# Kernel tuning notes

Hardware: AMD Instinct MI355X
Metric: run time of the kernel (lower is better)

The kernel has to match this reference:

```python
import jax, jax.numpy as jnp
import numpy as np
import math

B, S, E, H = 2, 2048, 1024, 16
D = E // H  # head_dim = 64
WINDOW = 512
EPS = 1e-5


def _layernorm(x, gamma, beta):
    mu = jnp.mean(x, axis=-1, keepdims=True)
    var = jnp.var(x, axis=-1, keepdims=True)
    return (x - mu) * jax.lax.rsqrt(var + EPS) * gamma + beta


def setup_inputs() -> dict:
    key = jax.random.key(0)
    ks = jax.random.split(key, 5)
    return {
        "x": jax.random.normal(ks[0], (B, S, E), jnp.float32),
        "W_qkv": jax.random.normal(ks[1], (E, 3 * E), jnp.float32) * (E ** -0.5),
        "b_qkv": jax.random.normal(ks[2], (3 * E,), jnp.float32) * 0.02,
        "q_gamma": jnp.ones((D,), jnp.float32),
        "q_beta": jnp.zeros((D,), jnp.float32),
        "k_gamma": jnp.ones((D,), jnp.float32),
        "k_beta": jnp.zeros((D,), jnp.float32),
        "W_out": jax.random.normal(ks[3], (E, E), jnp.float32) * (E ** -0.5),
        "b_out": jax.random.normal(ks[4], (E,), jnp.float32) * 0.02,
    }


def reference(x, W_qkv, b_qkv, q_gamma, q_beta, k_gamma, k_beta, W_out, b_out):
    b, s, e = x.shape
    # fused QKV projection -> (3, B, H, S, D)
    qkv = (x @ W_qkv + b_qkv).reshape(b, s, 3, H, D).transpose(2, 0, 3, 1, 4)
    q, k, v = qkv[0], qkv[1], qkv[2]
    # qk_norm: LayerNorm over head_dim
    q = _layernorm(q, q_gamma, q_beta)
    k = _layernorm(k, k_gamma, k_beta)
    scores = jnp.einsum("bhqd,bhkd->bhqk", q, k) / math.sqrt(D)
    # causal + sliding-window mask (True = masked out)
    row = jnp.arange(s)[:, None]
    col = jnp.arange(s)[None, :]
    masked = (col > row) | (row - col >= WINDOW)  # sliding window subsumes causal
    scores = jnp.where(masked[None, None], -jnp.inf, scores)
    attn = jax.nn.softmax(scores, axis=-1)
    out = jnp.einsum("bhqk,bhkd->bhqd", attn, v)  # (B,H,S,D)
    out = out.transpose(0, 2, 1, 3).reshape(b, s, e)
    return out @ W_out + b_out
```

## Files before the change

### kernel.cpp

```cpp
#include <hip/hip_runtime.h>
#include <stdint.h>

typedef uint16_t u16;
typedef __attribute__((ext_vector_type(8))) short short8;
typedef __attribute__((ext_vector_type(4))) float f32x4;

#define DEV static __device__ __forceinline__

DEV u16 f2bf(float f) {
  uint32_t u = __float_as_uint(f);
  return (u16)((u + 0x7fffu + ((u >> 16) & 1u)) >> 16);
}
DEV float bf2f(u16 h) { return __uint_as_float(((uint32_t)h) << 16); }

DEV void gload16(const void* g, void* l) {
  __builtin_amdgcn_global_load_lds(
      (const __attribute__((address_space(1))) void*)g,
      (__attribute__((address_space(3))) void*)l, 16, 0, 0);
}

__global__ void k_cast4(const float* __restrict__ in, u16* __restrict__ out, int n4) {
  int i = blockIdx.x * blockDim.x + threadIdx.x;
  if (i >= n4) return;
  float4 v = ((const float4*)in)[i];
  uint2 p;
  p.x = (uint32_t)f2bf(v.x) | ((uint32_t)f2bf(v.y) << 16);
  p.y = (uint32_t)f2bf(v.z) | ((uint32_t)f2bf(v.w) << 16);
  ((uint2*)out)[i] = p;
}

__global__ void k_tcast(const float* __restrict__ Wm, u16* __restrict__ Wt, int K, int N) {
  __shared__ u16 t[64][65];
  int n0 = blockIdx.x * 64, k0 = blockIdx.y * 64;
  int tid = threadIdx.x;
#pragma unroll
  for (int i = 0; i < 16; ++i) {
    int idx = tid + i * 256, r = idx >> 6, c = idx & 63;
    t[r][c] = f2bf(Wm[(size_t)(k0 + r) * N + n0 + c]);
  }
  __syncthreads();
#pragma unroll
  for (int i = 0; i < 16; ++i) {
    int idx = tid + i * 256, r = idx >> 6, c = idx & 63;
    Wt[(size_t)(n0 + r) * K + k0 + c] = t[c][r];
  }
}

__global__ __launch_bounds__(512) void k_gemmqkv8(
    const u16* __restrict__ A, const u16* __restrict__ Bt,
    const float* __restrict__ bias,
    const float* __restrict__ qg, const float* __restrict__ qb,
    const float* __restrict__ kg, const float* __restrict__ kb,
    u16* __restrict__ Qn, u16* __restrict__ Kn, u16* __restrict__ Vt) {
  const int K = 1024, N = 3072;
  __shared__ __attribute__((aligned(16))) u16 SA[2][16384];
  __shared__ __attribute__((aligned(16))) u16 SB[2][16384];
  int bid = blockIdx.x;
  int ntn = N >> 8;
  int cpx = gridDim.x >> 3;
  int wg = (bid & 7) * cpx + (bid >> 3);
  int my = wg / ntn, nx = wg - my * ntn;
  int m0 = my * 256, n0 = nx * 256;
  int tid = threadIdx.x, lane = tid & 63, w = tid >> 6;
  int wm = w >> 2, wn = w & 3;
  int wr = wm * 128, wc = wn * 64;
  int lr = lane & 15, lg = lane >> 4;
  int rsw = (lr & 7) << 3;
  int srow = tid >> 3;
  int scb = ((tid & 7) ^ ((tid >> 3) & 7)) * 8;
  f32x4 acc[8][4];
#pragma unroll
  for (int i = 0; i < 8; ++i)
#pragma unroll
    for (int j = 0; j < 4; ++j) acc[i][j] = (f32x4){0.f, 0.f, 0.f, 0.f};

  int nk = K >> 6;

#define STG8(buf, kt)                                                                    \
  do {                                                                                   \
    gload16(A + (size_t)(m0 + srow) * K + (kt) * 64 + scb, &SA[buf][tid * 8]);           \
    gload16(A + (size_t)(m0 + 64 + srow) * K + (kt) * 64 + scb, &SA[buf][4096 + tid * 8]);   \
    gload16(A + (size_t)(m0 + 128 + srow) * K + (kt) * 64 + scb, &SA[buf][8192 + tid * 8]);  \
    gload16(A + (size_t)(m0 + 192 + srow) * K + (kt) * 64 + scb, &SA[buf][12288 + tid * 8]); \
    gload16(Bt + (size_t)(n0 + srow) * K + (kt) * 64 + scb, &SB[buf][tid * 8]);          \
    gload16(Bt + (size_t)(n0 + 64 + srow) * K + (kt) * 64 + scb, &SB[buf][4096 + tid * 8]);  \
    gload16(Bt + (size_t)(n0 + 128 + srow) * K + (kt) * 64 + scb, &SB[buf][8192 + tid * 8]); \
    gload16(Bt + (size_t)(n0 + 192 + srow) * K + (kt) * 64 + scb, &SB[buf][12288 + tid * 8]); \
  } while (0)

  STG8(0, 0);
  STG8(1, 1);

  for (int t = 0; t < nk; ++t) {
    int cur = t & 1;
    if (t + 1 < nk)
      asm volatile("s_waitcnt vmcnt(8)" ::: "memory");
    else
      asm volatile("s_waitcnt vmcnt(0)" ::: "memory");
    __syncthreads();
#pragma unroll
    for (int ks = 0; ks < 2; ++ks) {
      short8 bfr[4];
#pragma unroll
      for (int ni = 0; ni < 4; ++ni)
        bfr[ni] = *(const short8*)&SB[cur][((wc + ni * 16 + lr) * 64 + ks * 32 + lg * 8) ^ rsw];
#pragma unroll
      for (int mh = 0; mh < 2; ++mh) {
        short8 afr[4];
#pragma unroll
        for (int a = 0; a < 4; ++a)
          afr[a] = *(const short8*)&SA[cur][((wr + (mh * 4 + a) * 16 + lr) * 64 + ks * 32 + lg * 8) ^ rsw];
        __builtin_amdgcn_s_setprio(1);
#pragma unroll
        for (int a = 0; a < 4; ++a)
#pragma unroll
          for (int ni = 0; ni < 4; ++ni)
            acc[mh * 4 + a][ni] =
                __builtin_amdgcn_mfma_f32_16x16x32_bf16(afr[a], bfr[ni], acc[mh * 4 + a][ni], 0, 0, 0);
        __builtin_amdgcn_s_setprio(0);
      }
    }
    __syncthreads();
    if (t + 2 < nk) STG8(cur, t + 2);
  }
#undef STG8

  int sec = n0 >> 10;
  int hh = ((n0 + wc) >> 6) & 15;
  int b = m0 >> 11;
  int s0 = m0 & 2047;

  if (sec < 2) {
    const float* gp = sec ? kg : qg;
    const float* bp = sec ? kb : qb;
    float scl = sec ? 1.f : (0.125f * 1.44269504f);
    u16* op = sec ? Kn : Qn;
    float gv[4], bev[4], bb[4];
#pragma unroll
    for (int ni = 0; ni < 4; ++ni) {
      int d = ni * 16 + lr;
      gv[ni] = gp[d];
      bev[ni] = bp[d];
      bb[ni] = bias[n0 + wc + d];
    }
    size_t hb = (size_t)(b * 16 + hh) * 2048 * 64;
#pragma unroll
    for (int mi = 0; mi < 8; ++mi) {
      float a[4][4], ps[4], ps2[4];
#pragma unroll
      for (int ni = 0; ni < 4; ++ni)
#pragma unroll
        for (int j = 0; j < 4; ++j) a[ni][j] = acc[mi][ni][j] + bb[ni];
#pragma unroll
      for (int j = 0; j < 4; ++j) {
        ps[j] = a[0][j] + a[1][j] + a[2][j] + a[3][j];
        ps2[j] = a[0][j] * a[0][j] + a[1][j] * a[1][j] + a[2][j] * a[2][j] + a[3][j] * a[3][j];
      }
#pragma unroll
      for (int m = 1; m < 16; m <<= 1)
#pragma unroll
        for (int j = 0; j < 4; ++j) {
          ps[j] += __shfl_xor(ps[j], m, 64);
          ps2[j] += __shfl_xor(ps2[j], m, 64);
        }
#pragma unroll
      for (int j = 0; j < 4; ++j) {
        float mean = ps[j] * (1.f / 64);
        float var = ps2[j] * (1.f / 64) - mean * mean;
        float r = rsqrtf(var + 1e-5f);
        int row = s0 + wr + mi * 16 + lg * 4 + j;
        size_t base = hb + (size_t)row * 64;
#pragma unroll
        for (int ni = 0; ni < 4; ++ni) {
          float v = ((a[ni][j] - mean) * r * gv[ni] + bev[ni]) * scl;
          op[base + ni * 16 + lr] = f2bf(v);
        }
      }
    }
  } else {
    u16* vbase = Vt + (size_t)(b * 16 + hh) * 64 * 2048;
#pragma unroll
    for (int ni = 0; ni < 4; ++ni) {
      int d = ni * 16 + lr;
      float bb = bias[n0 + wc + d];
#pragma unroll
      for (int mi = 0; mi < 8; ++mi) {
        int row0 = s0 + wr + mi * 16 + lg * 4;
        uint2 pk;
        pk.x = (uint32_t)f2bf(acc[mi][ni][0] + bb) | ((uint32_t)f2bf(acc[mi][ni][1] + bb) << 16);
        pk.y = (uint32_t)f2bf(acc[mi][ni][2] + bb) | ((uint32_t)f2bf(acc[mi][ni][3] + bb) << 16);
        *(uint2*)(vbase + (size_t)d * 2048 + row0) = pk;
      }
    }
  }
}

template <int OUT_BF16>
__global__ __launch_bounds__(256) void k_gemm4(
    const u16* __restrict__ A, const u16* __restrict__ Bt,
    const float* __restrict__ bias, void* __restrict__ Cout,
    int M, int N, int K) {
  __shared__ __attribute__((aligned(16))) u16 S[2][2][128 * 64];
  int bid = blockIdx.x;
  int ntn = N >> 7;
  int cpx = gridDim.x >> 3;
  int wg = (bid & 7) * cpx + (bid >> 3);
  int my = wg / ntn, nx = wg - my * ntn;
  int m0 = my * 128, n0 = nx * 128;
  int tid = threadIdx.x, lane = tid & 63, w = tid >> 6;
  int wr = (w >> 1) * 64, wc = (w & 1) * 64;
  int lr = lane & 15, lg = lane >> 4;
  int rsw = (lr & 7) << 3;
  int srow = tid >> 3;
  int scb = ((tid & 7) ^ ((tid >> 3) & 7)) * 8;
  f32x4 acc[4][4];
#pragma unroll
  for (int i = 0; i < 4; ++i)
#pragma unroll
    for (int j = 0; j < 4; ++j) acc[i][j] = (f32x4){0.f, 0.f, 0.f, 0.f};

  int nk = K >> 6;

#define STG4(buf, kt)                                                                   \
  do {                                                                                  \
    gload16(A + (size_t)(m0 + srow) * K + (kt) * 64 + scb, &S[buf][0][tid * 8]);        \
    gload16(A + (size_t)(m0 + 32 + srow) * K + (kt) * 64 + scb, &S[buf][0][2048 + tid * 8]);  \
    gload16(A + (size_t)(m0 + 64 + srow) * K + (kt) * 64 + scb, &S[buf][0][4096 + tid * 8]);  \
    gload16(A + (size_t)(m0 + 96 + srow) * K + (kt) * 64 + scb, &S[buf][0][6144 + tid * 8]);  \
    gload16(Bt + (size_t)(n0 + srow) * K + (kt) * 64 + scb, &S[buf][1][tid * 8]);       \
    gload16(Bt + (size_t)(n0 + 32 + srow) * K + (kt) * 64 + scb, &S[buf][1][2048 + tid * 8]); \
    gload16(Bt + (size_t)(n0 + 64 + srow) * K + (kt) * 64 + scb, &S[buf][1][4096 + tid * 8]); \
    gload16(Bt + (size_t)(n0 + 96 + srow) * K + (kt) * 64 + scb, &S[buf][1][6144 + tid * 8]); \
  } while (0)

  STG4(0, 0);
  asm volatile("s_waitcnt vmcnt(0)" ::: "memory");
  __syncthreads();

  for (int t = 0; t < nk; ++t) {
    int cur = t & 1;
    if (t + 1 < nk) STG4(cur ^ 1, t + 1);
#pragma unroll
    for (int ks = 0; ks < 2; ++ks) {
      short8 af[4], bf[4];
#pragma unroll
      for (int mi = 0; mi < 4; ++mi)
        af[mi] = *(const short8*)&S[cur][0][((wr + mi * 16 + lr) * 64 + ks * 32 + lg * 8) ^ rsw];
#pragma unroll
      for (int ni = 0; ni < 4; ++ni)
        bf[ni] = *(const short8*)&S[cur][1][((wc + ni * 16 + lr) * 64 + ks * 32 + lg * 8) ^ rsw];
      __builtin_amdgcn_s_setprio(1);
#pragma unroll
      for (int mi = 0; mi < 4; ++mi)
#pragma unroll
        for (int ni = 0; ni < 4; ++ni)
          acc[mi][ni] = __builtin_amdgcn_mfma_f32_16x16x32_bf16(af[mi], bf[ni], acc[mi][ni], 0, 0, 0);
      __builtin_amdgcn_s_setprio(0);
    }
    asm volatile("s_waitcnt vmcnt(0)" ::: "memory");
    __syncthreads();
  }
#undef STG4

  int rg = lg * 4;
#pragma unroll
  for (int mi = 0; mi < 4; ++mi) {
#pragma unroll
    for (int ni = 0; ni < 4; ++ni) {
      int col = n0 + wc + ni * 16 + lr;
      float bv = bias[col];
#pragma unroll
      for (int j = 0; j < 4; ++j) {
        int row = m0 + wr + mi * 16 + rg + j;
        float o = acc[mi][ni][j] + bv;
        if (OUT_BF16) ((u16*)Cout)[(size_t)row * N + col] = f2bf(o);
        else ((float*)Cout)[(size_t)row * N + col] = o;
      }
    }
  }
}

__global__ __launch_bounds__(256) void k_attn7(
    const u16* __restrict__ Qn, const u16* __restrict__ Kn,
    const u16* __restrict__ Vt, u16* __restrict__ attb) {
  __shared__ __attribute__((aligned(16))) u16 KL[2][4096];
  __shared__ __attribute__((aligned(16))) u16 VL[2][4096];
  __shared__ __attribute__((aligned(16))) u16 Pl[4][2304];
  int bid = blockIdx.x;
  int xcd = bid & 7, idx = bid >> 3;
  int bh = xcd * 4 + (idx & 3);
  int qb = 15 - (idx >> 2);
  int q0 = qb * 128;
  int tid = threadIdx.x, lane = tid & 63, w = tid >> 6;
  int ln15 = lane & 15, lg = lane >> 4;
  int qlo = q0 + w * 32;
  const u16* Qh = Qn + (size_t)bh * (2048 * 64);
  const u16* Kh = Kn + (size_t)bh * (2048 * 64);
  const u16* Vh = Vt + (size_t)bh * (64 * 2048);
  int rsw = (ln15 & 7) << 3;
  int srow = tid >> 3;
  int scb = ((tid & 7) ^ ((tid >> 3) & 7)) * 8;

  short8 qf[2][2];
#pragma unroll
  for (int qs = 0; qs < 2; ++qs)
#pragma unroll
    for (int h2 = 0; h2 < 2; ++h2)
      qf[qs][h2] = *(const short8*)(Qh + (size_t)(qlo + qs * 16 + ln15) * 64 + h2 * 32 + lg * 8);

  f32x4 oacc[2][4];
#pragma unroll
  for (int qs = 0; qs < 2; ++qs)
#pragma unroll
    for (int dt = 0; dt < 4; ++dt) oacc[qs][dt] = (f32x4){0.f, 0.f, 0.f, 0.f};
  float lwp[2][4];
#pragma unroll
  for (int qs = 0; qs < 2; ++qs)
#pragma unroll
    for (int j = 0; j < 4; ++j) lwp[qs][j] = 0.f;

  int t0 = q0 >= 512 ? (q0 - 511) >> 6 : 0;
  int t1 = (q0 + 127) >> 6;

#define STAGE_A7(buf, kt)                                                              \
  do {                                                                                 \
    const u16* Kt_ = Kh + (size_t)(kt) * 4096;                                         \
    gload16(Kt_ + (size_t)srow * 64 + scb, &KL[buf][tid * 8]);                         \
    gload16(Kt_ + (size_t)(srow + 32) * 64 + scb, &KL[buf][2048 + tid * 8]);           \
    const u16* Vt_ = Vh + (size_t)(kt) * 64;                                           \
    gload16(Vt_ + (size_t)srow * 2048 + scb, &VL[buf][tid * 8]);                       \
    gload16(Vt_ + (size_t)(srow + 32) * 2048 + scb, &VL[buf][2048 + tid * 8]);         \
  } while (0)

  STAGE_A7(0, t0);
  asm volatile("s_waitcnt vmcnt(0)" ::: "memory");
  __syncthreads();

  for (int t = t0; t <= t1; ++t) {
    int cur = (t - t0) & 1;
    if (t + 1 <= t1) STAGE_A7(cur ^ 1, t + 1);
    int kt6 = t * 64;
    if (kt6 <= qlo + 31 && kt6 + 63 >= qlo - 511) {
      short8 kf[4][2];
#pragma unroll
      for (int c = 0; c < 4; ++c)
#pragma unroll
        for (int h2 = 0; h2 < 2; ++h2)
          kf[c][h2] = *(const short8*)&KL[cur][((c * 16 + ln15) * 64 + h2 * 32 + lg * 8) ^ rsw];
      f32x4 sf[2][4];
      __builtin_amdgcn_s_setprio(1);
#pragma unroll
      for (int qs = 0; qs < 2; ++qs)
#pragma unroll
        for (int c = 0; c < 4; ++c) {
          f32x4 z = (f32x4){0.f, 0.f, 0.f, 0.f};
          z = __builtin_amdgcn_mfma_f32_16x16x32_bf16(qf[qs][0], kf[c][0], z, 0, 0, 0);
          sf[qs][c] = __builtin_amdgcn_mfma_f32_16x16x32_bf16(qf[qs][1], kf[c][1], z, 0, 0, 0);
        }
      __builtin_amdgcn_s_setprio(0);
      bool interior = (kt6 + 63 <= qlo) && (kt6 >= qlo - 480);
      if (interior) {
#pragma unroll
        for (int qs = 0; qs < 2; ++qs)
#pragma unroll
          for (int c = 0; c < 4; ++c)
#pragma unroll
            for (int j = 0; j < 4; ++j) {
              float p = __builtin_amdgcn_exp2f(sf[qs][c][j]);
              sf[qs][c][j] = p;
              lwp[qs][j] += p;
            }
      } else {
#pragma unroll
        for (int qs = 0; qs < 2; ++qs)
#pragma unroll
          for (int c = 0; c < 4; ++c) {
            int kk = kt6 + c * 16 + ln15;
#pragma unroll
            for (int j = 0; j < 4; ++j) {
              int q = qlo + qs * 16 + lg * 4 + j;
              bool msk = (kk > q) || ((q - kk) >= 512);
              float p = __builtin_amdgcn_exp2f(msk ? -1e30f : sf[qs][c][j]);
              sf[qs][c][j] = p;
              lwp[qs][j] += p;
            }
          }
      }
#pragma unroll
      for (int qs = 0; qs < 2; ++qs)
#pragma unroll
        for (int c = 0; c < 4; ++c)
#pragma unroll
          for (int j = 0; j < 4; ++j) {
            uint32_t u = __float_as_uint(sf[qs][c][j]);
            Pl[w][(qs * 16 + lg * 4 + j) * 72 + c * 16 + ln15] = (u16)((u + 0x8000u) >> 16);
          }
      short8 vf[4][2];
#pragma unroll
      for (int dt = 0; dt < 4; ++dt)
#pragma unroll
        for (int h2 = 0; h2 < 2; ++h2)
          vf[dt][h2] = *(const short8*)&VL[cur][((dt * 16 + ln15) * 64 + h2 * 32 + lg * 8) ^ rsw];
      __builtin_amdgcn_s_setprio(1);
#pragma unroll
      for (int qs = 0; qs < 2; ++qs)
#pragma unroll
        for (int h2 = 0; h2 < 2; ++h2) {
          short8 pf = *(const short8*)&Pl[w][(qs * 16 + ln15) * 72 + h2 * 32 + lg * 8];
#pragma unroll
          for (int dt = 0; dt < 4; ++dt)
            oacc[qs][dt] = __builtin_amdgcn_mfma_f32_16x16x32_bf16(pf, vf[dt][h2], oacc[qs][dt], 0, 0, 0);
        }
      __builtin_amdgcn_s_setprio(0);
    }
    asm volatile("s_waitcnt vmcnt(0)" ::: "memory");
    __syncthreads();
  }
#undef STAGE_A7

  int b = bh >> 4, hh = bh & 15;
#pragma unroll
  for (int qs = 0; qs < 2; ++qs)
#pragma unroll
    for (int j = 0; j < 4; ++j) {
      float rs = lwp[qs][j];
#pragma unroll
      for (int m = 8; m > 0; m >>= 1) rs += __shfl_xor(rs, m, 64);
      float inv = rs > 0.f ? 1.f / rs : 0.f;
      int row = b * 2048 + qlo + qs * 16 + lg * 4 + j;
#pragma unroll
      for (int dt = 0; dt < 4; ++dt)
        attb[(size_t)row * 1024 + hh * 64 + dt * 16 + ln15] = f2bf(oacc[qs][dt][j] * inv);
    }
}

extern "C" void kernel_launch(void* const* d_in, const int* in_sizes, int n_in,
                              void* d_out, int out_size, void* d_ws, size_t ws_size,
                              hipStream_t stream) {
  const float* x = (const float*)d_in[0];
  const float* Wqkv = (const float*)d_in[1];
  const float* bqkv = (const float*)d_in[2];
  const float* qg = (const float*)d_in[3];
  const float* qb = (const float*)d_in[4];
  const float* kg = (const float*)d_in[5];
  const float* kb = (const float*)d_in[6];
  const float* Wout = (const float*)d_in[7];
  const float* bout = (const float*)d_in[8];
  float* out = (float*)d_out;

  char* ws = (char*)d_ws;
  u16* attb = (u16*)(ws);
  u16* Vt = (u16*)(ws + 8388608);
  u16* Qn = (u16*)(ws + 16777216);
  u16* Kn = (u16*)(ws + 25165824);
  u16* xb = (u16*)(ws + 33554432);
  u16* wqkvT = (u16*)(ws + 41943040);
  u16* woutT = (u16*)(ws + 48234496);

  k_cast4<<<4096, 256, 0, stream>>>(x, xb, 4194304 / 4);
  k_tcast<<<dim3(48, 16), 256, 0, stream>>>(Wqkv, wqkvT, 1024, 3072);
  k_tcast<<<dim3(16, 16), 256, 0, stream>>>(Wout, woutT, 1024, 1024);
  k_gemmqkv8<<<192, 512, 0, stream>>>(xb, wqkvT, bqkv, qg, qb, kg, kb, Qn, Kn, Vt);
  k_attn7<<<512, 256, 0, stream>>>(Qn, Kn, Vt, attb);
  k_gemm4<0><<<256, 256, 0, stream>>>(attb, woutT, bout, out, 4096, 1024, 1024);
}
```

Before: 100.7 us.

## Restructure QKV GEMM main loop into 8-phase ping-pong pipeline

Replaces the simple double-buffered k-loop of the fused QKV GEMM with a hand-scheduled pipeline. Each k-tile is split into four quadrant MFMA phases. Shared-memory fragment loads, split global-to-LDS loads and raw s_barrier plus lgkmcnt waits are interleaved between the phases. The aim is to overlap memory traffic with MFMA work and hide barrier latency better. In exchange it adds many more barriers and hard-coded vmcnt counts, and buffer-reuse ordering races are a real risk.

```diff
diff --git a/kernel.cpp b/kernel.cpp
--- a/kernel.cpp
+++ b/kernel.cpp
@@ -46,7 +46,7 @@
   }
 }
 
-__global__ __launch_bounds__(512) void k_gemmqkv8(
+__global__ __launch_bounds__(512) void k_gemmqkv8p(
     const u16* __restrict__ A, const u16* __restrict__ Bt,
     const float* __restrict__ bias,
     const float* __restrict__ qg, const float* __restrict__ qb,
@@ -74,56 +74,84 @@
 #pragma unroll
     for (int j = 0; j < 4; ++j) acc[i][j] = (f32x4){0.f, 0.f, 0.f, 0.f};
 
-  int nk = K >> 6;
-
-#define STG8(buf, kt)                                                                    \
-  do {                                                                                   \
-    gload16(A + (size_t)(m0 + srow) * K + (kt) * 64 + scb, &SA[buf][tid * 8]);           \
-    gload16(A + (size_t)(m0 + 64 + srow) * K + (kt) * 64 + scb, &SA[buf][4096 + tid * 8]);   \
-    gload16(A + (size_t)(m0 + 128 + srow) * K + (kt) * 64 + scb, &SA[buf][8192 + tid * 8]);  \
-    gload16(A + (size_t)(m0 + 192 + srow) * K + (kt) * 64 + scb, &SA[buf][12288 + tid * 8]); \
-    gload16(Bt + (size_t)(n0 + srow) * K + (kt) * 64 + scb, &SB[buf][tid * 8]);          \
-    gload16(Bt + (size_t)(n0 + 64 + srow) * K + (kt) * 64 + scb, &SB[buf][4096 + tid * 8]);  \
-    gload16(Bt + (size_t)(n0 + 128 + srow) * K + (kt) * 64 + scb, &SB[buf][8192 + tid * 8]); \
-    gload16(Bt + (size_t)(n0 + 192 + srow) * K + (kt) * 64 + scb, &SB[buf][12288 + tid * 8]); \
-  } while (0)
-
-  STG8(0, 0);
-  STG8(1, 1);
-
-  for (int t = 0; t < nk; ++t) {
-    int cur = t & 1;
-    if (t + 1 < nk)
-      asm volatile("s_waitcnt vmcnt(8)" ::: "memory");
-    else
+#define STG_A0(buf, kt) { gload16(A + (size_t)(m0 + srow) * K + (kt) * 64 + scb, &SA[buf][tid * 8]); \
+                          gload16(A + (size_t)(m0 + 64 + srow) * K + (kt) * 64 + scb, &SA[buf][4096 + tid * 8]); }
+#define STG_A1(buf, kt) { gload16(A + (size_t)(m0 + 128 + srow) * K + (kt) * 64 + scb, &SA[buf][8192 + tid * 8]); \
+                          gload16(A + (size_t)(m0 + 192 + srow) * K + (kt) * 64 + scb, &SA[buf][12288 + tid * 8]); }
+#define STG_B0(buf, kt) { gload16(Bt + (size_t)(n0 + srow) * K + (kt) * 64 + scb, &SB[buf][tid * 8]); \
+                          gload16(Bt + (size_t)(n0 + 64 + srow) * K + (kt) * 64 + scb, &SB[buf][4096 + tid * 8]); }
+#define STG_B1(buf, kt) { gload16(Bt + (size_t)(n0 + 128 + srow) * K + (kt) * 64 + scb, &SB[buf][8192 + tid * 8]); \
+                          gload16(Bt + (size_t)(n0 + 192 + srow) * K + (kt) * 64 + scb, &SB[buf][12288 + tid * 8]); }
+
+  short8 afr[4][2], bfr[2][2];
+#define DSA8(BUF, MH)                                                         \
+  _Pragma("unroll") for (int a2 = 0; a2 < 4; ++a2)                            \
+  _Pragma("unroll") for (int ks = 0; ks < 2; ++ks)                            \
+    afr[a2][ks] = *(const short8*)&SA[BUF][((wr + (MH) * 64 + a2 * 16 + lr) * 64 + ks * 32 + lg * 8) ^ rsw];
+#define DSB4(BUF, NH)                                                         \
+  _Pragma("unroll") for (int n2 = 0; n2 < 2; ++n2)                            \
+  _Pragma("unroll") for (int ks = 0; ks < 2; ++ks)                            \
+    bfr[n2][ks] = *(const short8*)&SB[BUF][((wc + (NH) * 32 + n2 * 16 + lr) * 64 + ks * 32 + lg * 8) ^ rsw];
+#define MFMAQ(MH, NH)                                                         \
+  __builtin_amdgcn_s_setprio(1);                                              \
+  _Pragma("unroll") for (int ks = 0; ks < 2; ++ks)                            \
+  _Pragma("unroll") for (int a2 = 0; a2 < 4; ++a2)                            \
+  _Pragma("unroll") for (int n2 = 0; n2 < 2; ++n2)                            \
+    acc[(MH) * 4 + a2][(NH) * 2 + n2] = __builtin_amdgcn_mfma_f32_16x16x32_bf16( \
+        afr[a2][ks], bfr[n2][ks], acc[(MH) * 4 + a2][(NH) * 2 + n2], 0, 0, 0); \
+  __builtin_amdgcn_s_setprio(0);
+#define BAR1LG() { __builtin_amdgcn_s_barrier(); asm volatile("s_waitcnt lgkmcnt(0)" ::: "memory"); }
+#define BAR2()   { __builtin_amdgcn_s_barrier(); }
+
+  STG_A0(0, 0); STG_A1(0, 0); STG_B0(0, 0); STG_B1(0, 0);
+  STG_A0(1, 1); STG_A1(1, 1); STG_B0(1, 1); STG_B1(1, 1);
+  asm volatile("s_waitcnt vmcnt(8)" ::: "memory");
+  __builtin_amdgcn_s_barrier();
+
+  for (int i = 0; i < 8; ++i) {
+    int T1 = 2 * i + 1, T2 = 2 * i + 2, T3 = 2 * i + 3;
+    DSA8(0, 0); DSB4(0, 0);
+    if (i > 0) STG_A1(1, T1);
+    BAR1LG(); MFMAQ(0, 0); BAR2();
+    DSB4(0, 1);
+    if (i > 0) STG_B0(1, T1);
+    BAR1LG(); MFMAQ(0, 1); BAR2();
+    DSA8(0, 1);
+    if (i > 0) STG_B1(1, T1);
+    BAR1LG(); MFMAQ(1, 1); BAR2();
+    DSB4(0, 0);
+    if (i < 7) {
+      STG_A0(0, T2);
+      asm volatile("s_waitcnt vmcnt(2)" ::: "memory");
+    } else {
       asm volatile("s_waitcnt vmcnt(0)" ::: "memory");
-    __syncthreads();
-#pragma unroll
-    for (int ks = 0; ks < 2; ++ks) {
-      short8 bfr[4];
-#pragma unroll
-      for (int ni = 0; ni < 4; ++ni)
-        bfr[ni] = *(const short8*)&SB[cur][((wc + ni * 16 + lr) * 64 + ks * 32 + lg * 8) ^ rsw];
-#pragma unroll
-      for (int mh = 0; mh < 2; ++mh) {
-        short8 afr[4];
-#pragma unroll
-        for (int a = 0; a < 4; ++a)
-          afr[a] = *(const short8*)&SA[cur][((wr + (mh * 4 + a) * 16 + lr) * 64 + ks * 32 + lg * 8) ^ rsw];
-        __builtin_amdgcn_s_setprio(1);
-#pragma unroll
-        for (int a = 0; a < 4; ++a)
-#pragma unroll
-          for (int ni = 0; ni < 4; ++ni)
-            acc[mh * 4 + a][ni] =
-                __builtin_amdgcn_mfma_f32_16x16x32_bf16(afr[a], bfr[ni], acc[mh * 4 + a][ni], 0, 0, 0);
-        __builtin_amdgcn_s_setprio(0);
-      }
-    }
-    __syncthreads();
-    if (t + 2 < nk) STG8(cur, t + 2);
-  }
-#undef STG8
+    }
+    BAR1LG(); MFMAQ(1, 0); BAR2();
+    DSA8(1, 0); DSB4(1, 0);
+    if (i < 7) STG_A1(0, T2);
+    BAR1LG(); MFMAQ(0, 0); BAR2();
+    DSB4(1, 1);
+    if (i < 7) STG_B0(0, T2);
+    BAR1LG(); MFMAQ(0, 1); BAR2();
+    DSA8(1, 1);
+    if (i < 7) STG_B1(0, T2);
+    BAR1LG(); MFMAQ(1, 1); BAR2();
+    DSB4(1, 0);
+    if (i < 7) {
+      STG_A0(1, T3);
+      asm volatile("s_waitcnt vmcnt(2)" ::: "memory");
+    }
+    BAR1LG(); MFMAQ(1, 0); BAR2();
+  }
+#undef STG_A0
+#undef STG_A1
+#undef STG_B0
+#undef STG_B1
+#undef DSA8
+#undef DSB4
+#undef MFMAQ
+#undef BAR1LG
+#undef BAR2
 
   int sec = n0 >> 10;
   int hh = ((n0 + wc) >> 6) & 15;
@@ -460,7 +488,7 @@
   k_cast4<<<4096, 256, 0, stream>>>(x, xb, 4194304 / 4);
   k_tcast<<<dim3(48, 16), 256, 0, stream>>>(Wqkv, wqkvT, 1024, 3072);
   k_tcast<<<dim3(16, 16), 256, 0, stream>>>(Wout, woutT, 1024, 1024);
-  k_gemmqkv8<<<192, 512, 0, stream>>>(xb, wqkvT, bqkv, qg, qb, kg, kb, Qn, Kn, Vt);
+  k_gemmqkv8p<<<192, 512, 0, stream>>>(xb, wqkvT, bqkv, qg, qb, kg, kb, Qn, Kn, Vt);
   k_attn7<<<512, 256, 0, stream>>>(Qn, Kn, Vt, attb);
   k_gemm4<0><<<256, 256, 0, stream>>>(attb, woutT, bout, out, 4096, 1024, 1024);
 }
```

New measurement: 102.6 us. No clear change (+1.9%).
